# Optimization experiments

Measured on AMD Instinct MI355X. Metric: run time of the kernel, lower is better.

## Reference

```python
import jax, jax.numpy as jnp
import numpy as np

B, LQ, LK, D = 16, 2048, 2048, 256
NEG = -1e10


def setup_inputs() -> dict:
    key = jax.random.key(0)
    k1, k2, k3, k4, k5 = jax.random.split(key, 5)
    scale = 1.0 / np.sqrt(D)
    return {
        "x": jax.random.normal(k1, (B, LQ, D), dtype=jnp.float32),
        "y": jax.random.normal(k2, (B, LK, D), dtype=jnp.float32),
        "mask": jnp.zeros((B, LK), dtype=bool),  # True = padded key position
        "Wq": jax.random.normal(k3, (D, D), dtype=jnp.float32) * scale,
        "Wk": jax.random.normal(k4, (D, D), dtype=jnp.float32) * scale,
        "Wv": jax.random.normal(k5, (D, D), dtype=jnp.float32) * scale,
    }


def reference(x, y, mask, Wq, Wk, Wv):
    # nn.Linear: out = in @ W.T (no bias)
    q = jnp.einsum('bqd,ed->bqe', x, Wq)   # [B, LQ, D]
    k = jnp.einsum('bkd,ed->bke', y, Wk)   # [B, LK, D]
    v = jnp.einsum('bkd,ed->bke', y, Wv)   # [B, LK, D]
    # cdist (p=2) via GEMM expansion: ||q||^2 + ||k||^2 - 2 q.k
    qn = jnp.sum(q * q, axis=-1)                              # [B, LQ]
    kn = jnp.sum(k * k, axis=-1)                              # [B, LK]
    d2 = qn[:, :, None] + kn[:, None, :] - 2.0 * jnp.einsum('bqd,bkd->bqk', q, k)
    dist = jnp.sqrt(jnp.maximum(d2, 0.0))                     # [B, LQ, LK]
    scores = jnp.exp(-dist)
    # masked_fill: where original mask is True, set pre-softmax score to -1e10
    scores = jnp.where(mask[:, None, :], NEG, scores)
    attn = jax.nn.softmax(scores, axis=-1)                    # [B, LQ, LK]
    att_out = jnp.einsum('bqk,bkd->bqd', attn, v)             # [B, LQ, D]
    return (att_out, attn)
```

## Files before the change

### kernel.cpp

```cpp
#include <hip/hip_runtime.h>
#include <stdint.h>

#define B_   16
#define L_   2048
#define D_   256
#define NROW (B_*L_)

#define EPAD 40
#define TPAD 66

typedef __attribute__((ext_vector_type(8))) short s8v;
typedef __attribute__((ext_vector_type(4))) float f4v;

__device__ __forceinline__ unsigned short f2b(float f) {
    unsigned u = __builtin_bit_cast(unsigned, f);
    return (unsigned short)((u + 0x7fffu + ((u >> 16) & 1u)) >> 16);
}

__device__ __forceinline__ void gl16(const void* g, void* l) {
    __builtin_amdgcn_global_load_lds(
        (const __attribute__((address_space(1))) unsigned int*)g,
        (__attribute__((address_space(3))) unsigned int*)l, 16, 0, 0);
}

__global__ __launch_bounds__(256) void qkv_kernel(
    const float* __restrict__ x, const float* __restrict__ y,
    const float* __restrict__ Wq, const float* __restrict__ Wk, const float* __restrict__ Wv,
    unsigned short* __restrict__ Qb, unsigned short* __restrict__ Kb,
    unsigned short* __restrict__ Vt,
    float* __restrict__ qn, float* __restrict__ kn)
{
    __shared__ unsigned short Xs[64*256];
    __shared__ unsigned short Ws[64*256];
    __shared__ unsigned short Ts[64*TPAD];

    const int t    = threadIdx.x;
    const int r0   = blockIdx.x * 64;
    const int type = blockIdx.y;

    const float* X = type ? y : x;

    #pragma unroll
    for (int p = 0; p < 16; ++p) {
        int idx  = p*256 + t;
        int row  = idx >> 6;
        int half = idx & 1;
        int blk  = (idx & 63) >> 1;
        int c4   = blk*8 + half*4;
        float4 vx = *(const float4*)(X + (size_t)(r0+row)*D_ + c4);
        uint2 px;
        px.x = (unsigned)f2b(vx.x) | ((unsigned)f2b(vx.y) << 16);
        px.y = (unsigned)f2b(vx.z) | ((unsigned)f2b(vx.w) << 16);
        *(uint2*)(Xs + row*256 + (blk ^ (row & 15))*8 + half*4) = px;
    }

    const int w = t >> 6, lane = t & 63, q16 = lane & 15, quad = lane >> 4;
    const int m0 = w * 16;

    float p4[4] = {0.f, 0.f, 0.f, 0.f};
    const f4v z4 = {0.f, 0.f, 0.f, 0.f};

    for (int ct = 0; ct < 4; ++ct) {
        const int e0 = ct * 64;

        __syncthreads();
        {
            const float* W = type ? Wk : Wq;
            #pragma unroll
            for (int p = 0; p < 16; ++p) {
                int idx  = p*256 + t;
                int row  = idx >> 6;
                int half = idx & 1;
                int blk  = (idx & 63) >> 1;
                int c4   = blk*8 + half*4;
                float4 vw = *(const float4*)(W + (size_t)(e0+row)*D_ + c4);
                uint2 pw;
                pw.x = (unsigned)f2b(vw.x) | ((unsigned)f2b(vw.y) << 16);
                pw.y = (unsigned)f2b(vw.z) | ((unsigned)f2b(vw.w) << 16);
                *(uint2*)(Ws + row*256 + (blk ^ (row & 15))*8 + half*4) = pw;
            }
        }
        __syncthreads();

        f4v acc[4];
        #pragma unroll
        for (int n = 0; n < 4; ++n) acc[n] = z4;
        #pragma unroll
        for (int c = 0; c < 8; ++c) {
            s8v a = *(const s8v*)(Xs + (m0 + q16)*256 + (((c*4+quad) ^ q16)*8));
            #pragma unroll
            for (int n = 0; n < 4; ++n) {
                s8v bb = *(const s8v*)(Ws + (n*16 + q16)*256 + (((c*4+quad) ^ q16)*8));
                acc[n] = __builtin_amdgcn_mfma_f32_16x16x32_bf16(a, bb, acc[n], 0, 0, 0);
            }
        }
        {
            unsigned short* Out = type ? Kb : Qb;
            #pragma unroll
            for (int n = 0; n < 4; ++n)
                #pragma unroll
                for (int r = 0; r < 4; ++r) {
                    float v = acc[n][r];
                    p4[r] += v * v;
                    Out[(size_t)(r0 + m0 + quad*4 + r)*D_ + e0 + n*16 + q16] = f2b(v);
                }
        }

        if (type) {
            __syncthreads();
            #pragma unroll
            for (int p = 0; p < 16; ++p) {
                int idx  = p*256 + t;
                int row  = idx >> 6;
                int half = idx & 1;
                int blk  = (idx & 63) >> 1;
                int c4   = blk*8 + half*4;
                float4 vw = *(const float4*)(Wv + (size_t)(e0+row)*D_ + c4);
                uint2 pw;
                pw.x = (unsigned)f2b(vw.x) | ((unsigned)f2b(vw.y) << 16);
                pw.y = (unsigned)f2b(vw.z) | ((unsigned)f2b(vw.w) << 16);
                *(uint2*)(Ws + row*256 + (blk ^ (row & 15))*8 + half*4) = pw;
            }
            __syncthreads();

            f4v vacc[4];
            #pragma unroll
            for (int n = 0; n < 4; ++n) vacc[n] = z4;
            #pragma unroll
            for (int c = 0; c < 8; ++c) {
                s8v a = *(const s8v*)(Xs + (m0 + q16)*256 + (((c*4+quad) ^ q16)*8));
                #pragma unroll
                for (int n = 0; n < 4; ++n) {
                    s8v bb = *(const s8v*)(Ws + (n*16 + q16)*256 + (((c*4+quad) ^ q16)*8));
                    vacc[n] = __builtin_amdgcn_mfma_f32_16x16x32_bf16(a, bb, vacc[n], 0, 0, 0);
                }
            }
            #pragma unroll
            for (int n = 0; n < 4; ++n)
                #pragma unroll
                for (int r = 0; r < 4; ++r)
                    Ts[(m0 + quad*4 + r)*TPAD + n*16 + q16] = f2b(vacc[n][r]);
            __syncthreads();
            int j    = t >> 2;
            int kseg = t & 3;
            unsigned pk[8];
            #pragma unroll
            for (int i = 0; i < 8; ++i) {
                unsigned lo = Ts[(kseg*16 + 2*i    )*TPAD + j];
                unsigned hi = Ts[(kseg*16 + 2*i + 1)*TPAD + j];
                pk[i] = lo | (hi << 16);
            }
            int bb_ = r0 >> 11;
            int k0g = r0 & (L_ - 1);
            unsigned short* dst = Vt + (size_t)(bb_*D_ + e0 + j)*L_ + k0g + kseg*16;
            *(uint4*)dst       = make_uint4(pk[0], pk[1], pk[2], pk[3]);
            *((uint4*)dst + 1) = make_uint4(pk[4], pk[5], pk[6], pk[7]);
        }
    }

    {
        float* norm = type ? kn : qn;
        #pragma unroll
        for (int r = 0; r < 4; ++r) {
            float v = p4[r];
            v += __shfl_xor(v, 1, 16);
            v += __shfl_xor(v, 2, 16);
            v += __shfl_xor(v, 4, 16);
            v += __shfl_xor(v, 8, 16);
            if (q16 == 0) norm[r0 + m0 + quad*4 + r] = v;
        }
    }
}

__device__ __forceinline__ void stage_K(const unsigned short* Kb, unsigned short* ks,
                                        int bk, int k0, int w, int lane) {
    #pragma unroll
    for (int p = 0; p < 4; ++p) {
        int slot = p*256 + w*64 + lane;
        int row  = slot >> 5;
        int blk  = slot & 31;
        gl16(Kb + (size_t)(bk + k0 + row)*D_ + ((blk ^ (row & 15))*8),
             ks + (size_t)(p*256 + w*64)*8);
    }
}
__device__ __forceinline__ void stage_V(const unsigned short* Vt, unsigned short* vs,
                                        int bD, int k0, int w, int lane) {
    #pragma unroll
    for (int p = 0; p < 4; ++p) {
        int slot = p*256 + w*64 + lane;
        int d    = slot >> 2;
        int blk  = slot & 3;
        gl16(Vt + (size_t)(bD + d)*L_ + k0 + ((blk ^ ((d >> 1) & 3))*8),
             vs + (size_t)(p*256 + w*64)*8);
    }
}

__global__ __launch_bounds__(256) void attnpv_kernel(
    const unsigned short* __restrict__ Qb, const unsigned short* __restrict__ Kb,
    const unsigned short* __restrict__ Vt,
    const float* __restrict__ qn, const float* __restrict__ kn,
    const unsigned char* __restrict__ mask,
    unsigned short* __restrict__ Eb,
    float* __restrict__ rowsum, float* __restrict__ att_out)
{
    __shared__ unsigned short Ks[2][32*256];
    __shared__ unsigned short Vs[2][256*32];
    __shared__ unsigned short Es[4][16*EPAD];

    const int t  = threadIdx.x;
    const int q0 = blockIdx.x * 64;
    const int b  = blockIdx.y;
    const int bk = b * L_;
    const int bD = b * D_;
    const int w = t >> 6, lane = t & 63, q16 = lane & 15, quad = lane >> 4;

    const int qrow = bk + q0 + w*16;
    s8v qa[8];
    float qnr[4];
    #pragma unroll
    for (int c = 0; c < 8; ++c)
        qa[c] = *(const s8v*)(Qb + (size_t)(qrow + q16)*D_ + c*32 + quad*8);
    #pragma unroll
    for (int r = 0; r < 4; ++r)
        qnr[r] = qn[qrow + quad*4 + r];

    unsigned short* ebase = Eb + (size_t)(qrow + (lane >> 2))*L_ + (lane & 3)*8;
    const unsigned short* esrc = &Es[w][(lane >> 2)*EPAD + (lane & 3)*8];

    float rs[4] = {0.f, 0.f, 0.f, 0.f};
    const f4v z4 = {0.f, 0.f, 0.f, 0.f};
    f4v O[16];
    #pragma unroll
    for (int n = 0; n < 16; ++n) O[n] = z4;

    stage_K(Kb, Ks[0], bk, 0, w, lane);
    stage_V(Vt, Vs[0], bD, 0, w, lane);
    for (int kt = 0; kt < 64; ++kt) {
        const int k0 = kt * 32;
        const int cur = kt & 1;
        __syncthreads();
        if (kt < 63) {
            stage_K(Kb, Ks[cur ^ 1], bk, k0 + 32, w, lane);
            stage_V(Vt, Vs[cur ^ 1], bD, k0 + 32, w, lane);
        }

        float kcv[2]; int mkv[2];
        #pragma unroll
        for (int n = 0; n < 2; ++n) {
            kcv[n] = kn[bk + k0 + n*16 + q16];
            mkv[n] = mask[bk + k0 + n*16 + q16];
        }

        #pragma unroll
        for (int n = 0; n < 2; ++n) {
            f4v s = {0.f, 0.f, 0.f, 0.f};
            #pragma unroll
            for (int c = 0; c < 8; ++c) {
                s8v bb = *(const s8v*)(Ks[cur] + (n*16 + q16)*256 + (((c*4+quad) ^ q16)*8));
                s = __builtin_amdgcn_mfma_f32_16x16x32_bf16(qa[c], bb, s, 0, 0, 0);
            }
            #pragma unroll
            for (int r = 0; r < 4; ++r) {
                float d2 = qnr[r] + kcv[n] - 2.0f * s[r];
                float dist = sqrtf(fmaxf(d2, 0.f));
                float E = mkv[n] ? 0.f : __expf(__expf(-dist));
                rs[r] += E;
                Es[w][(quad*4 + r)*EPAD + n*16 + q16] = f2b(E);
            }
        }
        s8v af = *(const s8v*)(&Es[w][q16*EPAD + quad*8]);
        #pragma unroll
        for (int n = 0; n < 16; ++n) {
            s8v vb = *(const s8v*)(Vs[cur] + (n*16 + q16)*32 +
                                   ((quad ^ ((q16 >> 1) & 3))*8));
            O[n] = __builtin_amdgcn_mfma_f32_16x16x32_bf16(af, vb, O[n], 0, 0, 0);
        }
        *(s8v*)(ebase + k0) = *(const s8v*)esrc;
    }

    float inv[4];
    #pragma unroll
    for (int r = 0; r < 4; ++r) {
        float v = rs[r];
        v += __shfl_xor(v, 1, 16);
        v += __shfl_xor(v, 2, 16);
        v += __shfl_xor(v, 4, 16);
        v += __shfl_xor(v, 8, 16);
        if (q16 == 0) rowsum[qrow + quad*4 + r] = v;
        inv[r] = 1.0f / v;
    }

    #pragma unroll
    for (int n = 0; n < 16; ++n)
        #pragma unroll
        for (int r = 0; r < 4; ++r)
            att_out[(size_t)(qrow + quad*4 + r)*D_ + n*16 + q16] = O[n][r] * inv[r];
}

__global__ __launch_bounds__(256) void norm_kernel(
    const unsigned short* __restrict__ Eb,
    const float* __restrict__ rowsum,
    float* __restrict__ attn_out)
{
    const int row = blockIdx.x;
    const int t   = threadIdx.x;
    const float inv = 1.0f / rowsum[row];
    const size_t base = (size_t)row * L_ + t*8;

    s8v e = *(const s8v*)(Eb + base);
    float4 o0, o1;
    o0.x = __builtin_bit_cast(float, ((unsigned)(unsigned short)e[0]) << 16) * inv;
    o0.y = __builtin_bit_cast(float, ((unsigned)(unsigned short)e[1]) << 16) * inv;
    o0.z = __builtin_bit_cast(float, ((unsigned)(unsigned short)e[2]) << 16) * inv;
    o0.w = __builtin_bit_cast(float, ((unsigned)(unsigned short)e[3]) << 16) * inv;
    o1.x = __builtin_bit_cast(float, ((unsigned)(unsigned short)e[4]) << 16) * inv;
    o1.y = __builtin_bit_cast(float, ((unsigned)(unsigned short)e[5]) << 16) * inv;
    o1.z = __builtin_bit_cast(float, ((unsigned)(unsigned short)e[6]) << 16) * inv;
    o1.w = __builtin_bit_cast(float, ((unsigned)(unsigned short)e[7]) << 16) * inv;
    *(float4*)(attn_out + base)     = o0;
    *(float4*)(attn_out + base + 4) = o1;
}

extern "C" void kernel_launch(void* const* d_in, const int* in_sizes, int n_in,
                              void* d_out, int out_size, void* d_ws, size_t ws_size,
                              hipStream_t stream) {
    (void)in_sizes; (void)n_in; (void)out_size; (void)ws_size;
    const float* x  = (const float*)d_in[0];
    const float* y  = (const float*)d_in[1];
    const unsigned char* mask = (const unsigned char*)d_in[2];
    const float* Wq = (const float*)d_in[3];
    const float* Wk = (const float*)d_in[4];
    const float* Wv = (const float*)d_in[5];

    char* ws = (char*)d_ws;
    unsigned short* Qb = (unsigned short*)ws;
    unsigned short* Kb = Qb + (size_t)NROW * D_;
    unsigned short* Vt = Kb + (size_t)NROW * D_;
    float* qn     = (float*)(ws + 3 * (size_t)NROW * D_ * 2);
    float* kn     = qn + NROW;
    float* rowsum = kn + NROW;
    unsigned short* Eb = (unsigned short*)(rowsum + NROW);

    float* att_out = (float*)d_out;
    float* attn    = att_out + (size_t)NROW * D_;

    qkv_kernel<<<dim3(512, 2), 256, 0, stream>>>(x, y, Wq, Wk, Wv,
                                                 Qb, Kb, Vt, qn, kn);
    attnpv_kernel<<<dim3(32, 16), 256, 0, stream>>>(Qb, Kb, Vt, qn, kn, mask,
                                                    Eb, rowsum, att_out);
    norm_kernel<<<dim3(NROW), 256, 0, stream>>>(Eb, rowsum, attn);
}
```

Baseline: 590.7 us.

## Use 32x32 MFMA tiles in attention kernel and split V projection into own grid slice

The attention kernel switches from 16x16x32 to 32x32x16 bf16 MFMA with two waves of 32 query rows each (128 threads per block), which changes the register layout for scores, row sums and the output accumulator. K/V staging is reworked for the smaller block. The QKV projection kernel gets a third grid slice so V is computed by separate blocks instead of serially after K. This aims to raise MFMA efficiency and balance projection work, at the cost of fewer waves per block for hiding latency in the attention loop.

```diff
diff --git a/kernel.cpp b/kernel.cpp
--- a/kernel.cpp
+++ b/kernel.cpp
@@ -9,8 +9,9 @@
 #define EPAD 40
 #define TPAD 66
 
-typedef __attribute__((ext_vector_type(8))) short s8v;
-typedef __attribute__((ext_vector_type(4))) float f4v;
+typedef __attribute__((ext_vector_type(8)))  short s8v;
+typedef __attribute__((ext_vector_type(4)))  float f4v;
+typedef __attribute__((ext_vector_type(16))) float f16v;
 
 __device__ __forceinline__ unsigned short f2b(float f) {
     unsigned u = __builtin_bit_cast(unsigned, f);
@@ -38,7 +39,8 @@
     const int r0   = blockIdx.x * 64;
     const int type = blockIdx.y;
 
-    const float* X = type ? y : x;
+    const float* X = (type == 0) ? x : y;
+    const float* W = (type == 0) ? Wq : (type == 1) ? Wk : Wv;
 
     #pragma unroll
     for (int p = 0; p < 16; ++p) {
@@ -62,23 +64,19 @@
 
     for (int ct = 0; ct < 4; ++ct) {
         const int e0 = ct * 64;
-
         __syncthreads();
-        {
-            const float* W = type ? Wk : Wq;
-            #pragma unroll
-            for (int p = 0; p < 16; ++p) {
-                int idx  = p*256 + t;
-                int row  = idx >> 6;
-                int half = idx & 1;
-                int blk  = (idx & 63) >> 1;
-                int c4   = blk*8 + half*4;
-                float4 vw = *(const float4*)(W + (size_t)(e0+row)*D_ + c4);
-                uint2 pw;
-                pw.x = (unsigned)f2b(vw.x) | ((unsigned)f2b(vw.y) << 16);
-                pw.y = (unsigned)f2b(vw.z) | ((unsigned)f2b(vw.w) << 16);
-                *(uint2*)(Ws + row*256 + (blk ^ (row & 15))*8 + half*4) = pw;
-            }
+        #pragma unroll
+        for (int p = 0; p < 16; ++p) {
+            int idx  = p*256 + t;
+            int row  = idx >> 6;
+            int half = idx & 1;
+            int blk  = (idx & 63) >> 1;
+            int c4   = blk*8 + half*4;
+            float4 vw = *(const float4*)(W + (size_t)(e0+row)*D_ + c4);
+            uint2 pw;
+            pw.x = (unsigned)f2b(vw.x) | ((unsigned)f2b(vw.y) << 16);
+            pw.y = (unsigned)f2b(vw.z) | ((unsigned)f2b(vw.w) << 16);
+            *(uint2*)(Ws + row*256 + (blk ^ (row & 15))*8 + half*4) = pw;
         }
         __syncthreads();
 
@@ -94,8 +92,9 @@
                 acc[n] = __builtin_amdgcn_mfma_f32_16x16x32_bf16(a, bb, acc[n], 0, 0, 0);
             }
         }
-        {
-            unsigned short* Out = type ? Kb : Qb;
+
+        if (type < 2) {
+            unsigned short* Out = (type == 0) ? Qb : Kb;
             #pragma unroll
             for (int n = 0; n < 4; ++n)
                 #pragma unroll
@@ -104,42 +103,12 @@
                     p4[r] += v * v;
                     Out[(size_t)(r0 + m0 + quad*4 + r)*D_ + e0 + n*16 + q16] = f2b(v);
                 }
-        }
-
-        if (type) {
-            __syncthreads();
-            #pragma unroll
-            for (int p = 0; p < 16; ++p) {
-                int idx  = p*256 + t;
-                int row  = idx >> 6;
-                int half = idx & 1;
-                int blk  = (idx & 63) >> 1;
-                int c4   = blk*8 + half*4;
-                float4 vw = *(const float4*)(Wv + (size_t)(e0+row)*D_ + c4);
-                uint2 pw;
-                pw.x = (unsigned)f2b(vw.x) | ((unsigned)f2b(vw.y) << 16);
-                pw.y = (unsigned)f2b(vw.z) | ((unsigned)f2b(vw.w) << 16);
-                *(uint2*)(Ws + row*256 + (blk ^ (row & 15))*8 + half*4) = pw;
-            }
-            __syncthreads();
-
-            f4v vacc[4];
-            #pragma unroll
-            for (int n = 0; n < 4; ++n) vacc[n] = z4;
-            #pragma unroll
-            for (int c = 0; c < 8; ++c) {
-                s8v a = *(const s8v*)(Xs + (m0 + q16)*256 + (((c*4+quad) ^ q16)*8));
-                #pragma unroll
-                for (int n = 0; n < 4; ++n) {
-                    s8v bb = *(const s8v*)(Ws + (n*16 + q16)*256 + (((c*4+quad) ^ q16)*8));
-                    vacc[n] = __builtin_amdgcn_mfma_f32_16x16x32_bf16(a, bb, vacc[n], 0, 0, 0);
-                }
-            }
+        } else {
             #pragma unroll
             for (int n = 0; n < 4; ++n)
                 #pragma unroll
                 for (int r = 0; r < 4; ++r)
-                    Ts[(m0 + quad*4 + r)*TPAD + n*16 + q16] = f2b(vacc[n][r]);
+                    Ts[(m0 + quad*4 + r)*TPAD + n*16 + q16] = f2b(acc[n][r]);
             __syncthreads();
             int j    = t >> 2;
             int kseg = t & 3;
@@ -158,8 +127,8 @@
         }
     }
 
-    {
-        float* norm = type ? kn : qn;
+    if (type < 2) {
+        float* norm = (type == 0) ? qn : kn;
         #pragma unroll
         for (int r = 0; r < 4; ++r) {
             float v = p4[r];
@@ -175,27 +144,27 @@
 __device__ __forceinline__ void stage_K(const unsigned short* Kb, unsigned short* ks,
                                         int bk, int k0, int w, int lane) {
     #pragma unroll
-    for (int p = 0; p < 4; ++p) {
-        int slot = p*256 + w*64 + lane;
+    for (int p = 0; p < 8; ++p) {
+        int slot = p*128 + w*64 + lane;
         int row  = slot >> 5;
         int blk  = slot & 31;
         gl16(Kb + (size_t)(bk + k0 + row)*D_ + ((blk ^ (row & 15))*8),
-             ks + (size_t)(p*256 + w*64)*8);
+             ks + (size_t)(p*128 + w*64)*8);
     }
 }
 __device__ __forceinline__ void stage_V(const unsigned short* Vt, unsigned short* vs,
                                         int bD, int k0, int w, int lane) {
     #pragma unroll
-    for (int p = 0; p < 4; ++p) {
-        int slot = p*256 + w*64 + lane;
+    for (int p = 0; p < 8; ++p) {
+        int slot = p*128 + w*64 + lane;
         int d    = slot >> 2;
         int blk  = slot & 3;
         gl16(Vt + (size_t)(bD + d)*L_ + k0 + ((blk ^ ((d >> 1) & 3))*8),
-             vs + (size_t)(p*256 + w*64)*8);
-    }
-}
-
-__global__ __launch_bounds__(256) void attnpv_kernel(
+             vs + (size_t)(p*128 + w*64)*8);
+    }
+}
+
+__global__ __launch_bounds__(128) void attnpv_kernel(
     const unsigned short* __restrict__ Qb, const unsigned short* __restrict__ Kb,
     const unsigned short* __restrict__ Vt,
     const float* __restrict__ qn, const float* __restrict__ kn,
@@ -205,33 +174,41 @@
 {
     __shared__ unsigned short Ks[2][32*256];
     __shared__ unsigned short Vs[2][256*32];
-    __shared__ unsigned short Es[4][16*EPAD];
+    __shared__ unsigned short Es[2][32*EPAD];
 
     const int t  = threadIdx.x;
     const int q0 = blockIdx.x * 64;
     const int b  = blockIdx.y;
     const int bk = b * L_;
     const int bD = b * D_;
-    const int w = t >> 6, lane = t & 63, q16 = lane & 15, quad = lane >> 4;
-
-    const int qrow = bk + q0 + w*16;
-    s8v qa[8];
-    float qnr[4];
-    #pragma unroll
-    for (int c = 0; c < 8; ++c)
-        qa[c] = *(const s8v*)(Qb + (size_t)(qrow + q16)*D_ + c*32 + quad*8);
-    #pragma unroll
-    for (int r = 0; r < 4; ++r)
-        qnr[r] = qn[qrow + quad*4 + r];
-
-    unsigned short* ebase = Eb + (size_t)(qrow + (lane >> 2))*L_ + (lane & 3)*8;
-    const unsigned short* esrc = &Es[w][(lane >> 2)*EPAD + (lane & 3)*8];
-
-    float rs[4] = {0.f, 0.f, 0.f, 0.f};
-    const f4v z4 = {0.f, 0.f, 0.f, 0.f};
-    f4v O[16];
-    #pragma unroll
-    for (int n = 0; n < 16; ++n) O[n] = z4;
+    const int w    = t >> 6;
+    const int lane = t & 63;
+    const int col  = lane & 31;
+    const int h    = lane >> 5;
+
+    const int qrow = bk + q0 + w*32;
+
+    s8v qa[16];
+    #pragma unroll
+    for (int c = 0; c < 16; ++c)
+        qa[c] = *(const s8v*)(Qb + (size_t)(qrow + col)*D_ + c*16 + h*8);
+
+    float qnr[16];
+    #pragma unroll
+    for (int reg = 0; reg < 16; ++reg)
+        qnr[reg] = qn[qrow + (reg & 3) + 8*(reg >> 2) + 4*h];
+
+    unsigned short* ebase = Eb + (size_t)(qrow + (lane >> 1))*L_ + (lane & 1)*16;
+    const unsigned short* esrc = &Es[w][(lane >> 1)*EPAD + (lane & 1)*16];
+
+    float rs[16];
+    #pragma unroll
+    for (int reg = 0; reg < 16; ++reg) rs[reg] = 0.f;
+    f16v O[8];
+    #pragma unroll
+    for (int n = 0; n < 8; ++n)
+        #pragma unroll
+        for (int reg = 0; reg < 16; ++reg) O[n][reg] = 0.f;
 
     stage_K(Kb, Ks[0], bk, 0, w, lane);
     stage_V(Vt, Vs[0], bD, 0, w, lane);
@@ -244,57 +221,62 @@
             stage_V(Vt, Vs[cur ^ 1], bD, k0 + 32, w, lane);
         }
 
-        float kcv[2]; int mkv[2];
-        #pragma unroll
-        for (int n = 0; n < 2; ++n) {
-            kcv[n] = kn[bk + k0 + n*16 + q16];
-            mkv[n] = mask[bk + k0 + n*16 + q16];
-        }
-
-        #pragma unroll
-        for (int n = 0; n < 2; ++n) {
-            f4v s = {0.f, 0.f, 0.f, 0.f};
-            #pragma unroll
-            for (int c = 0; c < 8; ++c) {
-                s8v bb = *(const s8v*)(Ks[cur] + (n*16 + q16)*256 + (((c*4+quad) ^ q16)*8));
-                s = __builtin_amdgcn_mfma_f32_16x16x32_bf16(qa[c], bb, s, 0, 0, 0);
-            }
-            #pragma unroll
-            for (int r = 0; r < 4; ++r) {
-                float d2 = qnr[r] + kcv[n] - 2.0f * s[r];
-                float dist = sqrtf(fmaxf(d2, 0.f));
-                float E = mkv[n] ? 0.f : __expf(__expf(-dist));
-                rs[r] += E;
-                Es[w][(quad*4 + r)*EPAD + n*16 + q16] = f2b(E);
-            }
-        }
-        s8v af = *(const s8v*)(&Es[w][q16*EPAD + quad*8]);
-        #pragma unroll
-        for (int n = 0; n < 16; ++n) {
-            s8v vb = *(const s8v*)(Vs[cur] + (n*16 + q16)*32 +
-                                   ((quad ^ ((q16 >> 1) & 3))*8));
-            O[n] = __builtin_amdgcn_mfma_f32_16x16x32_bf16(af, vb, O[n], 0, 0, 0);
-        }
-        *(s8v*)(ebase + k0) = *(const s8v*)esrc;
-    }
-
-    float inv[4];
-    #pragma unroll
-    for (int r = 0; r < 4; ++r) {
-        float v = rs[r];
-        v += __shfl_xor(v, 1, 16);
-        v += __shfl_xor(v, 2, 16);
-        v += __shfl_xor(v, 4, 16);
-        v += __shfl_xor(v, 8, 16);
-        if (q16 == 0) rowsum[qrow + quad*4 + r] = v;
-        inv[r] = 1.0f / v;
-    }
-
-    #pragma unroll
-    for (int n = 0; n < 16; ++n)
-        #pragma unroll
-        for (int r = 0; r < 4; ++r)
-            att_out[(size_t)(qrow + quad*4 + r)*D_ + n*16 + q16] = O[n][r] * inv[r];
+        const float kc = kn[bk + k0 + col];
+        const int   mk = mask[bk + k0 + col];
+
+        f16v s;
+        #pragma unroll
+        for (int reg = 0; reg < 16; ++reg) s[reg] = 0.f;
+        #pragma unroll
+        for (int c = 0; c < 16; ++c) {
+            s8v bb = *(const s8v*)(Ks[cur] + col*256 + (((2*c + h) ^ (col & 15))*8));
+            s = __builtin_amdgcn_mfma_f32_32x32x16_bf16(qa[c], bb, s, 0, 0, 0);
+        }
+
+        #pragma unroll
+        for (int reg = 0; reg < 16; ++reg) {
+            float d2 = qnr[reg] + kc - 2.0f * s[reg];
+            float dist = __builtin_amdgcn_sqrtf(fmaxf(d2, 0.f));
+            float E = mk ? 0.f : __expf(__expf(-dist));
+            rs[reg] += E;
+            Es[w][((reg & 3) + 8*(reg >> 2) + 4*h)*EPAD + col] = f2b(E);
+        }
+
+        s8v af0 = *(const s8v*)(&Es[w][col*EPAD + h*8]);
+        s8v af1 = *(const s8v*)(&Es[w][col*EPAD + 16 + h*8]);
+        #pragma unroll
+        for (int n = 0; n < 8; ++n) {
+            int d  = n*32 + col;
+            int sw = (d >> 1) & 3;
+            s8v vb0 = *(const s8v*)(Vs[cur] + d*32 + ((h ^ sw)*8));
+            s8v vb1 = *(const s8v*)(Vs[cur] + d*32 + (((2 + h) ^ sw)*8));
+            O[n] = __builtin_amdgcn_mfma_f32_32x32x16_bf16(af0, vb0, O[n], 0, 0, 0);
+            O[n] = __builtin_amdgcn_mfma_f32_32x32x16_bf16(af1, vb1, O[n], 0, 0, 0);
+        }
+
+        *(s8v*)(ebase + k0)     = *(const s8v*)esrc;
+        *(s8v*)(ebase + k0 + 8) = *(const s8v*)(esrc + 8);
+    }
+
+    float inv[16];
+    #pragma unroll
+    for (int reg = 0; reg < 16; ++reg) {
+        float v = rs[reg];
+        v += __shfl_xor(v, 1, 32);
+        v += __shfl_xor(v, 2, 32);
+        v += __shfl_xor(v, 4, 32);
+        v += __shfl_xor(v, 8, 32);
+        v += __shfl_xor(v, 16, 32);
+        if (col == 0) rowsum[qrow + (reg & 3) + 8*(reg >> 2) + 4*h] = v;
+        inv[reg] = 1.0f / v;
+    }
+
+    #pragma unroll
+    for (int n = 0; n < 8; ++n)
+        #pragma unroll
+        for (int reg = 0; reg < 16; ++reg)
+            att_out[(size_t)(qrow + (reg & 3) + 8*(reg >> 2) + 4*h)*D_ + n*32 + col]
+                = O[n][reg] * inv[reg];
 }
 
 __global__ __launch_bounds__(256) void norm_kernel(
@@ -344,9 +326,9 @@
     float* att_out = (float*)d_out;
     float* attn    = att_out + (size_t)NROW * D_;
 
-    qkv_kernel<<<dim3(512, 2), 256, 0, stream>>>(x, y, Wq, Wk, Wv,
+    qkv_kernel<<<dim3(512, 3), 256, 0, stream>>>(x, y, Wq, Wk, Wv,
                                                  Qb, Kb, Vt, qn, kn);
-    attnpv_kernel<<<dim3(32, 16), 256, 0, stream>>>(Qb, Kb, Vt, qn, kn, mask,
+    attnpv_kernel<<<dim3(32, 16), 128, 0, stream>>>(Qb, Kb, Vt, qn, kn, mask,
                                                     Eb, rowsum, att_out);
     norm_kernel<<<dim3(NROW), 256, 0, stream>>>(Eb, rowsum, attn);
 }
```

After: 597.0 us. Within noise of the previous version (+1.1%).
